# Optimization experiments

Measured on AMD Instinct MI355X. Metric: run time of the kernel, lower is better.

Reference implementation:

```python
import jax, jax.numpy as jnp
import numpy as np

K = 4
TEMPERATURE = 34.0
OUT_CH = 256
KSIZE = 3
PAD = 1


def setup_inputs() -> dict:
    key = jax.random.key(0)
    ks = jax.random.split(key, 6)
    B, C, H, W = 16, 256, 56, 56
    hidden = int(C * 0.25) + 1  # 65
    x = jax.random.normal(ks[0], (B, C, H, W), dtype=jnp.float32)
    w_fc1 = jax.random.normal(ks[1], (hidden, C), dtype=jnp.float32) * (2.0 / C) ** 0.5
    w_fc2 = jax.random.normal(ks[2], (K, hidden), dtype=jnp.float32) * (2.0 / hidden) ** 0.5
    b_fc2 = jnp.zeros((K,), dtype=jnp.float32)
    weight = jax.random.normal(ks[3], (OUT_CH, C, KSIZE, KSIZE), dtype=jnp.float32) * 0.05
    bias = jax.random.normal(ks[4], (K, OUT_CH), dtype=jnp.float32) * 0.01
    return {"x": x, "w_fc1": w_fc1, "w_fc2": w_fc2, "b_fc2": b_fc2,
            "weight": weight, "bias": bias}


def _attention(x, w_fc1, w_fc2, b_fc2):
    pooled = x.mean(axis=(2, 3))                     # [B, C] adaptive avgpool(1)
    h = jax.nn.relu(pooled @ w_fc1.T)                # 1x1 conv == linear
    raw = h @ w_fc2.T + b_fc2                        # [B, K]
    # gradient_approximation: hard one-hot fwd, softmax(x/T) bwd (straight-through)
    hard = jax.nn.one_hot(jnp.argmax(raw, axis=1), raw.shape[1], dtype=raw.dtype)
    soft = jax.nn.softmax(raw / TEMPERATURE, axis=1)
    att = jax.lax.stop_gradient(hard - soft) + soft
    return att, raw


def _quantize_banks(weight):
    # WDoReFaQuantizer with 'modified' scheme, bits 2..K+1, STE on the round step
    w = weight.reshape(-1)
    t = jnp.tanh(w)
    xq = t / jnp.max(jnp.abs(t))
    xq = (xq + 1.0) * 0.5                            # in [0, 1]
    banks = []
    for bit in range(2, 2 + K):
        a = float(1 << bit)
        q = jnp.minimum(jnp.floor(a * xq), a - 1.0) / a
        q = jax.lax.stop_gradient(q - xq) + xq       # STE: identity backward
        banks.append(q * 2.0 - 1.0)
    return jnp.stack(banks)                          # [K, O*C*k*k]


def reference(x, w_fc1, w_fc2, b_fc2, weight, bias):
    B, C, H, W = x.shape
    att, raw = _attention(x, w_fc1, w_fc2, b_fc2)    # [B, K], [B, K]
    wq = _quantize_banks(weight)                     # [K, N]
    agg_w = (att @ wq).reshape(B, OUT_CH, C, KSIZE, KSIZE)
    agg_b = att @ bias                               # [B, OUT_CH]

    def conv1(xi, wi):  # xi: [C,H,W], wi: [O,C,k,k]
        return jax.lax.conv_general_dilated(
            xi[None], wi, window_strides=(1, 1),
            padding=[(PAD, PAD), (PAD, PAD)],
            dimension_numbers=("NCHW", "OIHW", "NCHW"))[0]

    out = jax.vmap(conv1)(x, agg_w) + agg_b[:, :, None, None]
    return (out, raw)
```

## Files before the change

kernel.cpp:

```cpp
#include <hip/hip_runtime.h>
#include <math.h>

#define NB 16
#define NC 256
#define NH 56
#define NW 56
#define NHW 3136
#define NHID 65
#define NK 4
#define NOC 256
#define WN 589824
#define OUT0 12845056

#define WS_POOLED 0
#define WS_KB     4096
#define WS_MAX    4112
#define WS_MAXP   4128
#define WS_WQF    8192
#define WQB_OFF   32768ul
#define XP_OFF    4751360ul
#define WS_NEED   32325632ul

typedef unsigned int u32;
typedef unsigned short u16;
typedef unsigned long long u64;
typedef __attribute__((ext_vector_type(8))) short s8v;
typedef __attribute__((ext_vector_type(16))) float f16v;

__device__ __forceinline__ u16 f2bf(float f) {
    union { float f; u32 u; } v; v.f = f;
    u32 u = v.u;
    return (u16)((u + 0x7fffu + ((u >> 16) & 1u)) >> 16);
}

__device__ __forceinline__ void gload_lds16(const void* g, void* l) {
    __builtin_amdgcn_global_load_lds((const __attribute__((address_space(1))) u32*)g,
                                     (__attribute__((address_space(3))) u32*)l, 16, 0, 0);
}


__global__ __launch_bounds__(256) void k_prep(const float* __restrict__ x,
                                              const float* __restrict__ w,
                                              float* __restrict__ ws,
                                              float* __restrict__ scratch) {
    const int tid = threadIdx.x;
    if (blockIdx.x >= 896) {
        int j = blockIdx.x - 896;
        float m = 0.f;
        for (int i = j * 256 + tid; i < WN; i += 65536)
            m = fmaxf(m, fabsf(tanhf(w[i])));
        for (int off = 32; off > 0; off >>= 1) m = fmaxf(m, __shfl_down(m, off, 64));
        __shared__ float part[4];
        int lane = tid & 63, wv = tid >> 6;
        if (lane == 0) part[wv] = m;
        __syncthreads();
        if (tid == 0)
            ws[WS_MAXP + j] = fmaxf(fmaxf(part[0], part[1]), fmaxf(part[2], part[3]));
        return;
    }
    const int by = blockIdx.x;
    const int b = by / 56, y = by % 56;
    const int c16 = tid >> 4, q = tid & 15;
    __shared__ __align__(8) u16 Lbt[56 * 264];
    __shared__ float pl[256];
    u16* xp = (u16*)((char*)ws + XP_OFF);

    #pragma unroll
    for (int ci = 0; ci < 16; ++ci) {
        int c = ci * 16 + c16;
        float4 v = make_float4(0.f, 0.f, 0.f, 0.f);
        if (q < 14) {
            v = *(const float4*)(x + ((size_t)(b * 256 + c)) * NHW + (size_t)y * 56 + q * 4);
            Lbt[(q * 4 + 0) * 264 + c] = f2bf(v.x);
            Lbt[(q * 4 + 1) * 264 + c] = f2bf(v.y);
            Lbt[(q * 4 + 2) * 264 + c] = f2bf(v.z);
            Lbt[(q * 4 + 3) * 264 + c] = f2bf(v.w);
        }
        float s = v.x + v.y + v.z + v.w;
        s += __shfl_down(s, 8, 16);
        s += __shfl_down(s, 4, 16);
        s += __shfl_down(s, 2, 16);
        s += __shfl_down(s, 1, 16);
        if (q == 0) pl[c] = s;
    }
    __syncthreads();
    scratch[(size_t)by * 256 + tid] = pl[tid];
    u64* rowp = (u64*)xp + (size_t)(b * 58 + y + 1) * (58 * 64);
    for (int idx = tid; idx < 58 * 64; idx += 256) {
        int col = idx >> 6, cp = idx & 63;
        u64 v = 0ull;
        if (col >= 1 && col <= 56)
            v = *(const u64*)(Lbt + (col - 1) * 264 + cp * 4);
        rowp[idx] = v;
    }
    if (y == 0 || y == 55) {
        int row = (y == 0) ? 0 : 57;
        u64* brow = (u64*)xp + (size_t)(b * 58 + row) * (58 * 64);
        for (int idx = tid; idx < 58 * 64; idx += 256) brow[idx] = 0ull;
    }
}

__global__ __launch_bounds__(256) void k_mid(const float* __restrict__ w_fc1,
                                             const float* __restrict__ w_fc2,
                                             const float* __restrict__ b_fc2,
                                             const float* __restrict__ w,
                                             float* __restrict__ ws,
                                             const float* __restrict__ scratch,
                                             float* __restrict__ out_raw) {
    const int tid = threadIdx.x;
    if (blockIdx.x < 16) {
        const int b = blockIdx.x;
        __shared__ float pl[NC];
        __shared__ float hs[NHID];
        __shared__ float raws[NK];
        float p = 0.f;
        for (int y = 0; y < 56; ++y)
            p += scratch[((size_t)(b * 56 + y)) * 256 + tid];
        pl[tid] = p * (1.0f / NHW);
        __syncthreads();
        if (tid < NHID) {
            float s = 0.f;
            for (int c = 0; c < NC; ++c) s = fmaf(pl[c], w_fc1[tid * NC + c], s);
            hs[tid] = fmaxf(s, 0.f);
        }
        __syncthreads();
        if (tid < NK) {
            float s = b_fc2[tid];
            for (int j = 0; j < NHID; ++j) s = fmaf(hs[j], w_fc2[tid * NHID + j], s);
            raws[tid] = s;
            out_raw[b * NK + tid] = s;
        }
        __syncthreads();
        if (tid == 0) {
            int best = 0;
            for (int k = 1; k < NK; ++k) if (raws[k] > raws[best]) best = k;
            ((int*)(ws + WS_KB))[b] = best;
        }
        return;
    }
    __shared__ float mred[4];
    float mv = ws[WS_MAXP + tid];
    for (int off = 32; off > 0; off >>= 1) mv = fmaxf(mv, __shfl_down(mv, off, 64));
    if ((tid & 63) == 0) mred[tid >> 6] = mv;
    __syncthreads();
    const float maxt = fmaxf(fmaxf(mred[0], mred[1]), fmaxf(mred[2], mred[3]));

    u16* wqp = (u16*)((char*)ws + WQB_OFF);
    int idx = (blockIdx.x - 16) * 256 + tid;
    int o = idx >> 7, c2 = idx & 127;
    int ch0 = c2 * 2;
    int cs = ch0 >> 5, cc = ch0 & 31;
    int ks2 = cc >> 4, hf = (cc >> 3) & 1, j = cc & 7;
    int n = o & 31, ot = o >> 5;
    const float* wp = w + ((size_t)o * 256 + ch0) * 9;
    float t0[9], t1[9];
    #pragma unroll
    for (int t = 0; t < 9; ++t) t0[t] = tanhf(wp[t]);
    #pragma unroll
    for (int t = 0; t < 9; ++t) t1[t] = tanhf(wp[9 + t]);
    #pragma unroll
    for (int bank = 0; bank < 4; ++bank) {
        float a = (float)(4 << bank);
        #pragma unroll
        for (int tap = 0; tap < 9; ++tap) {
            float xq0 = (t0[tap] / maxt + 1.f) * 0.5f;
            float xq1 = (t1[tap] / maxt + 1.f) * 0.5f;
            float q0 = fminf(floorf(a * xq0), a - 1.f) / a * 2.f - 1.f;
            float q1 = fminf(floorf(a * xq1), a - 1.f) / a * 2.f - 1.f;
            u32 pk = (u32)f2bf(q0) | ((u32)f2bf(q1) << 16);
            size_t off16 = ((((size_t)((bank * 8 + ot) * 8 + cs)) * 18 + tap * 2 + ks2) * 64
                            + hf * 32 + n) * 8 + j;
            *(u32*)(wqp + off16) = pk;
        }
    }
}

__global__ __launch_bounds__(512, 4) void k_conv_mfma(const float* __restrict__ bias,
                                                      const float* __restrict__ ws_f,
                                                      float* __restrict__ out) {
    const int L = blockIdx.x;
    const int xcd = L & 7, slot = L >> 3;
    const int oq = slot >> 4;
    const int pair = xcd * 16 + (slot & 15);
    const int b = pair >> 3, strip = pair & 7;
    const int r0 = strip * 7;
    const int tid = threadIdx.x;
    const int wv = tid >> 6, lane = tid & 63;
    const int n = lane & 31, hf = lane >> 5;
    const int vw = (wv + (slot & 7)) & 7;
    const int ntile = (vw < 5) ? 2 : 1;
    const int t0 = (vw < 5) ? vw * 2 : 10 + (vw - 5);
    const int kb = ((const int*)(ws_f + WS_KB))[b];
    const u16* wqp = (const u16*)((const char*)ws_f + WQB_OFF);
    const u16* xp  = (const u16*)((const char*)ws_f + XP_OFF);

    __shared__ __align__(16) u16 Xl[2][18432];

    int bofs[2];
    #pragma unroll
    for (int t = 0; t < 2; ++t) {
        int p = (t0 + t) * 32 + n;
        if (t >= ntile || p > 391) p = 391;
        int pr = p / 56, pc = p - pr * 56;
        bofs[t] = pr * 4096 + hf * 1024 + pc * 16;
    }
    const int colc = (lane < 58) ? lane : 57;
    const u16* xsrc = xp + (((size_t)(b * 58 + r0)) * 58 + colc) * 256;
    const u16* ab0 = wqp + (size_t)((kb * 8 + oq * 2 + 0) * 8) * (18 * 64 * 8);
    const u16* ab1 = wqp + (size_t)((kb * 8 + oq * 2 + 1) * 8) * (18 * 64 * 8);

    f16v acc0[2], acc1[2];
    #pragma unroll
    for (int t = 0; t < 2; ++t) { acc0[t] = (f16v)0.f; acc1[t] = (f16v)0.f; }

    const int sbase = (wv < 4) ? wv * 5 : 20 + (wv - 4) * 4;
    const int scnt  = (wv < 4) ? 5 : 4;
    #pragma unroll
    for (int i = 0; i < 5; ++i)
        if (i < scnt) {
            int seg = sbase + i;
            gload_lds16(xsrc + (size_t)(seg >> 2) * (58 * 256) + (seg & 3) * 8,
                        (void*)(&Xl[0][seg * 512]));
        }
    __syncthreads();

    #pragma unroll 1
    for (int cs = 0; cs < 8; ++cs) {
        int pb = cs & 1;
        if (cs < 7) {
            int c0n = (cs + 1) * 32;
            #pragma unroll
            for (int i = 0; i < 5; ++i)
                if (i < scnt) {
                    int seg = sbase + i;
                    gload_lds16(xsrc + (size_t)(seg >> 2) * (58 * 256) + (seg & 3) * 8 + c0n,
                                (void*)(&Xl[pb ^ 1][seg * 512]));
                }
        }
        const u16* ap0 = ab0 + (size_t)cs * (18 * 64 * 8);
        const u16* ap1 = ab1 + (size_t)cs * (18 * 64 * 8);
        const char* XB = (const char*)&Xl[pb][0];
        #pragma unroll
        for (int r = 0; r < 3; ++r)
            #pragma unroll
            for (int s = 0; s < 3; ++s)
                #pragma unroll
                for (int ks = 0; ks < 2; ++ks) {
                    const int f = r * 6 + s * 2 + ks;
                    s8v a0 = *(const s8v*)(ap0 + (size_t)(f * 64 + lane) * 8);
                    s8v a1 = *(const s8v*)(ap1 + (size_t)(f * 64 + lane) * 8);
                    const int coff = r * 4096 + ks * 2048 + s * 16;
                    #pragma unroll
                    for (int t = 0; t < 2; ++t)
                        if (t < ntile) {
                            s8v bf = *(const s8v*)(XB + bofs[t] + coff);
                            acc0[t] = __builtin_amdgcn_mfma_f32_32x32x16_bf16(a0, bf, acc0[t], 0, 0, 0);
                            acc1[t] = __builtin_amdgcn_mfma_f32_32x32x16_bf16(a1, bf, acc1[t], 0, 0, 0);
                        }
                }
        __syncthreads();
    }

    #pragma unroll
    for (int t = 0; t < 2; ++t)
        if (t < ntile) {
            int p = (t0 + t) * 32 + n;
            if (p < 392) {
                int pr = p / 56, pc = p - pr * 56;
                float* op = out + (size_t)b * 256 * NHW + (size_t)(r0 + pr) * 56 + pc;
                #pragma unroll
                for (int reg = 0; reg < 16; ++reg) {
                    int m = (reg & 3) + 8 * (reg >> 2) + 4 * hf;
                    int o0 = oq * 64 + m;
                    op[(size_t)o0 * NHW] = acc0[t][reg] + bias[kb * NOC + o0];
                    op[(size_t)(o0 + 32) * NHW] = acc1[t][reg] + bias[kb * NOC + o0 + 32];
                }
            }
        }
}


__global__ __launch_bounds__(256) void k_pool(const float* __restrict__ x,
                                              float* __restrict__ ws) {
    int plane = blockIdx.x;
    const float* p = x + (size_t)plane * NHW;
    float s = 0.f;
    for (int i = threadIdx.x; i < NHW; i += 256) s += p[i];
    for (int off = 32; off > 0; off >>= 1) s += __shfl_down(s, off, 64);
    __shared__ float part[4];
    int lane = threadIdx.x & 63, wv = threadIdx.x >> 6;
    if (lane == 0) part[wv] = s;
    __syncthreads();
    if (threadIdx.x == 0)
        ws[WS_POOLED + plane] = part[0] + part[1] + part[2] + part[3];
}

__global__ __launch_bounds__(256) void k_fc(const float* __restrict__ w_fc1,
                                            const float* __restrict__ w_fc2,
                                            const float* __restrict__ b_fc2,
                                            float* __restrict__ ws,
                                            float* __restrict__ out_raw) {
    __shared__ float pl[NB * NC];
    __shared__ float hs[NB][NHID];
    __shared__ float raws[NB][NK];
    for (int i = threadIdx.x; i < NB * NC; i += 256)
        pl[i] = ws[WS_POOLED + i] * (1.0f / NHW);
    __syncthreads();
    for (int idx = threadIdx.x; idx < NB * NHID; idx += 256) {
        int b = idx / NHID, j = idx % NHID;
        float s = 0.f;
        for (int c = 0; c < NC; ++c) s = fmaf(pl[b * NC + c], w_fc1[j * NC + c], s);
        hs[b][j] = fmaxf(s, 0.f);
    }
    __syncthreads();
    if (threadIdx.x < NB * NK) {
        int b = threadIdx.x / NK, k = threadIdx.x % NK;
        float s = b_fc2[k];
        for (int j = 0; j < NHID; ++j) s = fmaf(hs[b][j], w_fc2[k * NHID + j], s);
        raws[b][k] = s;
        out_raw[b * NK + k] = s;
    }
    __syncthreads();
    if (threadIdx.x < NB) {
        int best = 0;
        for (int k = 1; k < NK; ++k)
            if (raws[threadIdx.x][k] > raws[threadIdx.x][best]) best = k;
        ((int*)(ws + WS_KB))[threadIdx.x] = best;
    }
}

__global__ __launch_bounds__(256) void k_maxtanh(const float* __restrict__ w,
                                                 float* __restrict__ ws) {
    float m = 0.f;
    for (int i = blockIdx.x * 256 + threadIdx.x; i < WN; i += gridDim.x * 256)
        m = fmaxf(m, fabsf(tanhf(w[i])));
    for (int off = 32; off > 0; off >>= 1) m = fmaxf(m, __shfl_down(m, off, 64));
    __shared__ float part[4];
    int lane = threadIdx.x & 63, wv = threadIdx.x >> 6;
    if (lane == 0) part[wv] = m;
    __syncthreads();
    if (threadIdx.x == 0) {
        float t = fmaxf(fmaxf(part[0], part[1]), fmaxf(part[2], part[3]));
        atomicMax((unsigned int*)ws + WS_MAX, __float_as_uint(t));
    }
}

__global__ __launch_bounds__(256) void k_quant(const float* __restrict__ w,
                                               float* __restrict__ ws) {
    float maxt = __uint_as_float(((const unsigned int*)ws)[WS_MAX]);
    float* wqf = ws + WS_WQF;
    for (int i = blockIdx.x * 256 + threadIdx.x; i < WN; i += gridDim.x * 256) {
        float t = tanhf(w[i]);
        float xq = (t / maxt + 1.0f) * 0.5f;
        #pragma unroll
        for (int k = 0; k < NK; ++k) {
            float a = (float)(4 << k);
            float q = fminf(floorf(a * xq), a - 1.0f) / a;
            wqf[(size_t)k * WN + i] = q * 2.0f - 1.0f;
        }
    }
}

__global__ __launch_bounds__(256) void k_conv(const float* __restrict__ x,
                                              const float* __restrict__ bias,
                                              const float* __restrict__ ws,
                                              float* __restrict__ out) {
    const int o_base = blockIdx.x * 16;
    const int row_base = blockIdx.y * 7;
    const int b = blockIdx.z;
    const int tid = threadIdx.x;
    const int w = tid & 63;
    const int og = tid >> 6;
    const int wc = (w < 56) ? w : 55;
    const int kb = ((const int*)(ws + WS_KB))[b];
    const float* wqf = ws + WS_WQF + (size_t)kb * WN;

    __shared__ float Xl[8][9][58];
    __shared__ float Wl[16][72];

    float acc[4][7];
    #pragma unroll
    for (int i = 0; i < 4; ++i)
        #pragma unroll
        for (int j = 0; j < 7; ++j) acc[i][j] = 0.f;

    for (int c0 = 0; c0 < NC; c0 += 8) {
        for (int idx = tid; idx < 1152; idx += 256) {
            int o = idx / 72, rem = idx - o * 72;
            Wl[o][rem] = wqf[(size_t)(o_base + o) * 2304 + c0 * 9 + rem];
        }
        for (int idx = tid; idx < 4176; idx += 256) {
            int c = idx / 522, rem = idx - c * 522;
            int ly = rem / 58, lx = rem - ly * 58;
            int gy = row_base - 1 + ly, gx = lx - 1;
            float v = 0.f;
            if (gy >= 0 && gy < NH && (unsigned)gx < (unsigned)NW)
                v = x[(((size_t)b * NC + c0 + c) * NH + gy) * NW + gx];
            Xl[c][ly][lx] = v;
        }
        __syncthreads();
        #pragma unroll 1
        for (int c = 0; c < 8; ++c) {
            float xv[9][3];
            #pragma unroll
            for (int ly = 0; ly < 9; ++ly)
                #pragma unroll
                for (int s = 0; s < 3; ++s)
                    xv[ly][s] = Xl[c][ly][wc + s];
            float wvv[4][9];
            #pragma unroll
            for (int i = 0; i < 4; ++i)
                #pragma unroll
                for (int t = 0; t < 9; ++t)
                    wvv[i][t] = Wl[og * 4 + i][c * 9 + t];
            #pragma unroll
            for (int i = 0; i < 4; ++i)
                #pragma unroll
                for (int j = 0; j < 7; ++j)
                    #pragma unroll
                    for (int r = 0; r < 3; ++r)
                        #pragma unroll
                        for (int s = 0; s < 3; ++s)
                            acc[i][j] = fmaf(wvv[i][r * 3 + s], xv[j + r][s], acc[i][j]);
        }
        __syncthreads();
    }

    if (w < 56) {
        #pragma unroll
        for (int i = 0; i < 4; ++i) {
            int o = o_base + og * 4 + i;
            float bb = bias[kb * NOC + o];
            #pragma unroll
            for (int j = 0; j < 7; ++j)
                out[(((size_t)b * NOC + o) * NH + (row_base + j)) * NW + w] = acc[i][j] + bb;
        }
    }
}

extern "C" void kernel_launch(void* const* d_in, const int* in_sizes, int n_in,
                              void* d_out, int out_size, void* d_ws, size_t ws_size,
                              hipStream_t stream) {
    const float* x      = (const float*)d_in[0];
    const float* w_fc1  = (const float*)d_in[1];
    const float* w_fc2  = (const float*)d_in[2];
    const float* b_fc2  = (const float*)d_in[3];
    const float* weight = (const float*)d_in[4];
    const float* bias   = (const float*)d_in[5];
    float* out = (float*)d_out;
    float* ws  = (float*)d_ws;

    if (ws_size >= WS_NEED) {
        hipLaunchKernelGGL(k_prep, dim3(1152), dim3(256), 0, stream, x, weight, ws, out);
        hipLaunchKernelGGL(k_mid, dim3(144), dim3(256), 0, stream,
                           w_fc1, w_fc2, b_fc2, weight, ws, out, out + OUT0);
        hipLaunchKernelGGL(k_conv_mfma, dim3(512), dim3(512), 0, stream, bias, ws, out);
    } else {
        hipLaunchKernelGGL(k_pool, dim3(NB * NC), dim3(256), 0, stream, x, ws);
        hipLaunchKernelGGL(k_fc, dim3(1), dim3(256), 0, stream,
                           w_fc1, w_fc2, b_fc2, ws, out + OUT0);
        hipLaunchKernelGGL(k_maxtanh, dim3(256), dim3(256), 0, stream, weight, ws);
        hipLaunchKernelGGL(k_quant, dim3(512), dim3(256), 0, stream, weight, ws);
        hipLaunchKernelGGL(k_conv, dim3(16, 8, NB), dim3(256), 0, stream, x, bias, ws, out);
    }
}
```

Measured before the change: 207.4 us.

## Stage weight fragments in LDS and halve workgroup size with more tiles per wave

The conv MFMA kernel goes from 512 to 256 threads per block. Each wave now computes 3–4 pixel tiles instead of 1–2, which gives more reuse of each A fragment per wave. Weight (A) fragments are now staged into LDS through double-buffered async loads alongside the input slab, instead of being read straight from global memory inside the MFMA loop. The K loop is split into 16 half-channel stages to fit the smaller LDS buffers. This raises register pressure (8 accumulator tiles) and adds more barriers per block.

Measured after the change: 186.1 us. 10.3% less time.

```diff
diff --git a/kernel.cpp b/kernel.cpp
--- a/kernel.cpp
+++ b/kernel.cpp
@@ -175,7 +175,7 @@
     }
 }
 
-__global__ __launch_bounds__(512, 4) void k_conv_mfma(const float* __restrict__ bias,
+__global__ __launch_bounds__(256, 2) void k_conv_mfma(const float* __restrict__ bias,
                                                       const float* __restrict__ ws_f,
                                                       float* __restrict__ out) {
     const int L = blockIdx.x;
@@ -187,83 +187,83 @@
     const int tid = threadIdx.x;
     const int wv = tid >> 6, lane = tid & 63;
     const int n = lane & 31, hf = lane >> 5;
-    const int vw = (wv + (slot & 7)) & 7;
-    const int ntile = (vw < 5) ? 2 : 1;
-    const int t0 = (vw < 5) ? vw * 2 : 10 + (vw - 5);
+    const int vw = (wv + (slot & 3)) & 3;
+    const int nt = (vw == 0) ? 4 : 3;
+    const int t0 = (vw == 0) ? 0 : 4 + (vw - 1) * 3;
     const int kb = ((const int*)(ws_f + WS_KB))[b];
     const u16* wqp = (const u16*)((const char*)ws_f + WQB_OFF);
     const u16* xp  = (const u16*)((const char*)ws_f + XP_OFF);
 
-    __shared__ __align__(16) u16 Xl[2][18432];
-
-    int bofs[2];
-    #pragma unroll
-    for (int t = 0; t < 2; ++t) {
+    __shared__ __align__(16) u16 Xl[2][9216];
+    __shared__ __align__(16) u16 Al[2][9216];
+
+    int bofs[4];
+    #pragma unroll
+    for (int t = 0; t < 4; ++t) {
         int p = (t0 + t) * 32 + n;
-        if (t >= ntile || p > 391) p = 391;
+        if (t >= nt || p > 391) p = 391;
         int pr = p / 56, pc = p - pr * 56;
-        bofs[t] = pr * 4096 + hf * 1024 + pc * 16;
+        bofs[t] = pr * 2048 + hf * 1024 + pc * 16;
     }
     const int colc = (lane < 58) ? lane : 57;
     const u16* xsrc = xp + (((size_t)(b * 58 + r0)) * 58 + colc) * 256;
     const u16* ab0 = wqp + (size_t)((kb * 8 + oq * 2 + 0) * 8) * (18 * 64 * 8);
     const u16* ab1 = wqp + (size_t)((kb * 8 + oq * 2 + 1) * 8) * (18 * 64 * 8);
 
-    f16v acc0[2], acc1[2];
-    #pragma unroll
-    for (int t = 0; t < 2; ++t) { acc0[t] = (f16v)0.f; acc1[t] = (f16v)0.f; }
-
-    const int sbase = (wv < 4) ? wv * 5 : 20 + (wv - 4) * 4;
-    const int scnt  = (wv < 4) ? 5 : 4;
-    #pragma unroll
-    for (int i = 0; i < 5; ++i)
-        if (i < scnt) {
-            int seg = sbase + i;
-            gload_lds16(xsrc + (size_t)(seg >> 2) * (58 * 256) + (seg & 3) * 8,
-                        (void*)(&Xl[0][seg * 512]));
-        }
+    f16v acc0[4], acc1[4];
+    #pragma unroll
+    for (int t = 0; t < 4; ++t) { acc0[t] = (f16v)0.f; acc1[t] = (f16v)0.f; }
+
+#define STAGE(stn, bn)                                                                   \
+    {                                                                                    \
+        const int csn = (stn) >> 1, ksn = (stn) & 1;                                     \
+        _Pragma("unroll")                                                                \
+        for (int i = 0; i < 9; ++i) {                                                    \
+            int seg = wv * 9 + i;                                                        \
+            if (seg < 18) {                                                              \
+                gload_lds16(xsrc + (size_t)(seg >> 1) * (58 * 256) + (stn) * 16 + (seg & 1) * 8, \
+                            (void*)(&Xl[bn][seg * 512]));                                \
+            } else {                                                                     \
+                int aa = seg - 18;                                                       \
+                int tile = (aa >= 9) ? 1 : 0;                                            \
+                int tap = aa - tile * 9;                                                 \
+                const u16* ab = tile ? ab1 : ab0;                                        \
+                gload_lds16(ab + (size_t)(csn * 18 + tap * 2 + ksn) * 512 + lane * 8,    \
+                            (void*)(&Al[bn][aa * 512]));                                 \
+            }                                                                            \
+        }                                                                                \
+    }
+
+    STAGE(0, 0);
     __syncthreads();
 
     #pragma unroll 1
-    for (int cs = 0; cs < 8; ++cs) {
-        int pb = cs & 1;
-        if (cs < 7) {
-            int c0n = (cs + 1) * 32;
-            #pragma unroll
-            for (int i = 0; i < 5; ++i)
-                if (i < scnt) {
-                    int seg = sbase + i;
-                    gload_lds16(xsrc + (size_t)(seg >> 2) * (58 * 256) + (seg & 3) * 8 + c0n,
-                                (void*)(&Xl[pb ^ 1][seg * 512]));
-                }
-        }
-        const u16* ap0 = ab0 + (size_t)cs * (18 * 64 * 8);
-        const u16* ap1 = ab1 + (size_t)cs * (18 * 64 * 8);
+    for (int st = 0; st < 16; ++st) {
+        int pb = st & 1;
+        if (st < 15) STAGE(st + 1, pb ^ 1);
+        const u16* AB = &Al[pb][0];
         const char* XB = (const char*)&Xl[pb][0];
         #pragma unroll
-        for (int r = 0; r < 3; ++r)
+        for (int tap = 0; tap < 9; ++tap) {
+            s8v a0 = *(const s8v*)(AB + tap * 512 + lane * 8);
+            s8v a1 = *(const s8v*)(AB + (9 + tap) * 512 + lane * 8);
+            const int r = tap / 3, s = tap % 3;
+            const int coff = r * 2048 + s * 16;
             #pragma unroll
-            for (int s = 0; s < 3; ++s)
-                #pragma unroll
-                for (int ks = 0; ks < 2; ++ks) {
-                    const int f = r * 6 + s * 2 + ks;
-                    s8v a0 = *(const s8v*)(ap0 + (size_t)(f * 64 + lane) * 8);
-                    s8v a1 = *(const s8v*)(ap1 + (size_t)(f * 64 + lane) * 8);
-                    const int coff = r * 4096 + ks * 2048 + s * 16;
-                    #pragma unroll
-                    for (int t = 0; t < 2; ++t)
-                        if (t < ntile) {
-                            s8v bf = *(const s8v*)(XB + bofs[t] + coff);
-                            acc0[t] = __builtin_amdgcn_mfma_f32_32x32x16_bf16(a0, bf, acc0[t], 0, 0, 0);
-                            acc1[t] = __builtin_amdgcn_mfma_f32_32x32x16_bf16(a1, bf, acc1[t], 0, 0, 0);
-                        }
+            for (int t = 0; t < 4; ++t)
+                if (t < nt) {
+                    s8v bf = *(const s8v*)(XB + bofs[t] + coff);
+                    acc0[t] = __builtin_amdgcn_mfma_f32_32x32x16_bf16(a0, bf, acc0[t], 0, 0, 0);
+                    acc1[t] = __builtin_amdgcn_mfma_f32_32x32x16_bf16(a1, bf, acc1[t], 0, 0, 0);
                 }
-        __syncthreads();
-    }
-
-    #pragma unroll
-    for (int t = 0; t < 2; ++t)
-        if (t < ntile) {
+        }
+        __syncthreads();
+    }
+#undef STAGE
+
+    #pragma unroll
+    for (int t = 0; t < 4; ++t)
+        if (t < nt) {
             int p = (t0 + t) * 32 + n;
             if (p < 392) {
                 int pr = p / 56, pc = p - pr * 56;
@@ -454,7 +454,7 @@
         hipLaunchKernelGGL(k_prep, dim3(1152), dim3(256), 0, stream, x, weight, ws, out);
         hipLaunchKernelGGL(k_mid, dim3(144), dim3(256), 0, stream,
                            w_fc1, w_fc2, b_fc2, weight, ws, out, out + OUT0);
-        hipLaunchKernelGGL(k_conv_mfma, dim3(512), dim3(512), 0, stream, bias, ws, out);
+        hipLaunchKernelGGL(k_conv_mfma, dim3(512), dim3(256), 0, stream, bias, ws, out);
     } else {
         hipLaunchKernelGGL(k_pool, dim3(NB * NC), dim3(256), 0, stream, x, ws);
         hipLaunchKernelGGL(k_fc, dim3(1), dim3(256), 0, stream,
```
